# Optimization experiments

Measured on AMD Instinct MI355X. Metric: run time of the kernel, lower is better.

The kernel has to match this reference:

```python
import jax, jax.numpy as jnp
import numpy as np

C = 256; G = 8; K = 3; P = K * K; GC = C // G
PAD = K // 2; PAD_DW = 1
EPS_LN = 1e-5; EPS_DWLN = 1e-6; EPS_BN = 1e-5
OFFSET_SCALE = 1.0


def _ln(x, g, b, eps=EPS_LN):
    mu = x.mean(-1, keepdims=True)
    var = ((x - mu) ** 2).mean(-1, keepdims=True)
    return (x - mu) * jax.lax.rsqrt(var + eps) * g + b


def _bn(x, g, b, m, v):  # x: NCHW, eval-mode batchnorm with running stats
    s = jax.lax.rsqrt(v + EPS_BN)
    return (x - m[None, :, None, None]) * (g * s)[None, :, None, None] + b[None, :, None, None]


def _dcnv3_core(x, offset, mask):
    # x: (N,H,W,C) projected input; offset: (N,H,W,G*P*2); mask: (N,H,W,G,P) softmaxed
    N, H, W, _ = x.shape
    Hp, Wp = H + 2 * PAD, W + 2 * PAD
    x_pad = jnp.pad(x, ((0, 0), (PAD, PAD), (PAD, PAD), (0, 0)))
    img = x_pad.reshape(N, Hp, Wp, G, GC).transpose(0, 3, 4, 1, 2)  # (N,G,gc,Hp,Wp)
    # reference points, normalized by padded spatial dims (stride=1, dilation=1)
    start = (K - 1) // 2 + 0.5
    ref_x = (start + jnp.arange(W, dtype=x.dtype)) / Wp
    ref_y = (start + jnp.arange(H, dtype=x.dtype)) / Hp
    rx, ry = jnp.meshgrid(ref_x, ref_y, indexing='xy')  # (H,W)
    ref = jnp.stack([rx, ry], -1)  # (H,W,2) as (x,y)
    # dilation grid (kernel tap offsets), tap index p = i_w*K + j_h per torch meshgrid order
    gw = (jnp.arange(K, dtype=x.dtype) - (K - 1) // 2) / Wp
    gh = (jnp.arange(K, dtype=x.dtype) - (K - 1) // 2) / Hp
    gxx, gyy = jnp.meshgrid(gw, gh, indexing='ij')
    grid = jnp.stack([gxx, gyy], -1).reshape(P, 2)
    norm = jnp.array([Wp, Hp], dtype=x.dtype)
    off = offset.reshape(N, H, W, G, P, 2) * (OFFSET_SCALE / norm)
    loc = ref[None, :, :, None, None, :] + grid * OFFSET_SCALE + off  # (N,H,W,G,P,2)
    sg = (2.0 * loc - 1.0).transpose(0, 3, 1, 2, 4, 5).reshape(N, G, H * W, P, 2)

    def sample_one(im, gr):  # im: (gc,Hp,Wp), gr: (HW,P,2) in [-1,1]
        gx = (gr[..., 0] + 1.0) * (Wp / 2) - 0.5  # align_corners=False
        gy = (gr[..., 1] + 1.0) * (Hp / 2) - 0.5
        x0 = jnp.floor(gx); y0 = jnp.floor(gy)
        wx = gx - x0; wy = gy - y0
        def gat(ix, iy):
            valid = ((ix >= 0) & (ix <= Wp - 1) & (iy >= 0) & (iy <= Hp - 1)).astype(im.dtype)
            ixc = jnp.clip(ix, 0, Wp - 1).astype(jnp.int32)
            iyc = jnp.clip(iy, 0, Hp - 1).astype(jnp.int32)
            return im[:, iyc, ixc] * valid  # (gc,HW,P), zero padding outside
        return (gat(x0, y0) * ((1 - wx) * (1 - wy))
                + gat(x0 + 1, y0) * (wx * (1 - wy))
                + gat(x0, y0 + 1) * ((1 - wx) * wy)
                + gat(x0 + 1, y0 + 1) * (wx * wy))

    sampled = jax.vmap(jax.vmap(sample_one))(img, sg)  # (N,G,gc,HW,P)
    m = mask.transpose(0, 3, 1, 2, 4).reshape(N, G, 1, H * W, P)
    out = (sampled * m).sum(-1)  # (N,G,gc,HW)
    return out.transpose(0, 3, 1, 2).reshape(N, H, W, C)


def _dcnv3(inp, dw_w, dw_b, dwln_g, dwln_b, off_w, off_b, msk_w, msk_b, inp_w, inp_b, outp_w, outp_b):
    N, H, W, _ = inp.shape
    x = inp @ inp_w + inp_b  # input_proj
    # depthwise conv offset/mask branch (on the raw input, not the projection)
    x1 = jax.lax.conv_general_dilated(inp, dw_w, (1, 1), ((PAD_DW, PAD_DW), (PAD_DW, PAD_DW)),
                                      dimension_numbers=('NHWC', 'HWIO', 'NHWC'),
                                      feature_group_count=C) + dw_b
    x1 = jax.nn.gelu(_ln(x1, dwln_g, dwln_b, EPS_DWLN), approximate=False)
    offset = x1 @ off_w + off_b  # (N,H,W,G*P*2)
    mask = jax.nn.softmax((x1 @ msk_w + msk_b).reshape(N, H, W, G, P), axis=-1)
    return _dcnv3_core(x, offset, mask) @ outp_w + outp_b  # output_proj


def _forward(x, conv1_w, bn1_g, bn1_b, bn1_m, bn1_v, ln1_g, ln1_b, dw_w, dw_b, dwln_g, dwln_b,
             off_w, off_b, msk_w, msk_b, inp_w, inp_b, outp_w, outp_b, gamma1,
             ln2_g, ln2_b, fc1_w, fc1_b, fc2_w, fc2_b, gamma2, bn2_g, bn2_b, bn2_m, bn2_v):
    out = jax.lax.conv_general_dilated(x, conv1_w, (1, 1), ((1, 1), (1, 1)),
                                       dimension_numbers=('NCHW', 'OIHW', 'NCHW'))
    out = jax.nn.relu(_bn(out, bn1_g, bn1_b, bn1_m, bn1_v))
    t = out.transpose(0, 2, 3, 1)  # NHWC for the InternImage layer
    # post_norm InternImage layer with layer_scale
    d = _dcnv3(t, dw_w, dw_b, dwln_g, dwln_b, off_w, off_b, msk_w, msk_b, inp_w, inp_b, outp_w, outp_b)
    t = t + gamma1 * _ln(d, ln1_g, ln1_b)
    h = jax.nn.gelu(t @ fc1_w + fc1_b, approximate=False) @ fc2_w + fc2_b
    t = t + gamma2 * _ln(h, ln2_g, ln2_b)
    out = _bn(t.transpose(0, 3, 1, 2), bn2_g, bn2_b, bn2_m, bn2_v)
    return jax.nn.relu(out + x)  # residual (downsample is None: stride=1, inplanes==planes)


def setup_inputs() -> dict:
    key = jax.random.key(0)
    ks = iter(jax.random.split(key, 48))
    rn = lambda shape, s=1.0: jax.random.normal(next(ks), shape, dtype=jnp.float32) * s
    hid = 4 * C
    d = {}
    d['x'] = rn((8, C, 56, 56))
    d['conv1_w'] = rn((C, C, 3, 3), (2.0 / (9 * C)) ** 0.5)
    d['bn1_g'] = jnp.ones((C,), jnp.float32); d['bn1_b'] = jnp.zeros((C,), jnp.float32)
    d['bn1_m'] = rn((C,), 0.1)
    d['bn1_v'] = jax.random.uniform(next(ks), (C,), jnp.float32, 0.5, 1.5)
    d['ln1_g'] = jnp.ones((C,), jnp.float32); d['ln1_b'] = jnp.zeros((C,), jnp.float32)
    d['dw_w'] = rn((3, 3, 1, C), (1.0 / 9) ** 0.5); d['dw_b'] = jnp.zeros((C,), jnp.float32)
    d['dwln_g'] = jnp.ones((C,), jnp.float32); d['dwln_b'] = jnp.zeros((C,), jnp.float32)
    d['off_w'] = rn((C, G * P * 2), 0.01); d['off_b'] = rn((G * P * 2,), 0.01)
    d['msk_w'] = rn((C, G * P), 0.01); d['msk_b'] = jnp.zeros((G * P,), jnp.float32)
    d['inp_w'] = rn((C, C), C ** -0.5); d['inp_b'] = jnp.zeros((C,), jnp.float32)
    d['outp_w'] = rn((C, C), C ** -0.5); d['outp_b'] = jnp.zeros((C,), jnp.float32)
    d['gamma1'] = rn((C,), 0.01)
    d['ln2_g'] = jnp.ones((C,), jnp.float32); d['ln2_b'] = jnp.zeros((C,), jnp.float32)
    d['fc1_w'] = rn((C, hid), C ** -0.5); d['fc1_b'] = jnp.zeros((hid,), jnp.float32)
    d['fc2_w'] = rn((hid, C), hid ** -0.5); d['fc2_b'] = jnp.zeros((C,), jnp.float32)
    d['gamma2'] = rn((C,), 0.01)
    d['bn2_g'] = jnp.ones((C,), jnp.float32); d['bn2_b'] = jnp.zeros((C,), jnp.float32)
    d['bn2_m'] = rn((C,), 0.1)
    d['bn2_v'] = jax.random.uniform(next(ks), (C,), jnp.float32, 0.5, 1.5)
    return d


def reference(x, conv1_w, bn1_g, bn1_b, bn1_m, bn1_v, ln1_g, ln1_b, dw_w, dw_b, dwln_g, dwln_b,
              off_w, off_b, msk_w, msk_b, inp_w, inp_b, outp_w, outp_b, gamma1,
              ln2_g, ln2_b, fc1_w, fc1_b, fc2_w, fc2_b, gamma2, bn2_g, bn2_b, bn2_m, bn2_v):
    return _forward(x, conv1_w, bn1_g, bn1_b, bn1_m, bn1_v, ln1_g, ln1_b, dw_w, dw_b, dwln_g, dwln_b,
                    off_w, off_b, msk_w, msk_b, inp_w, inp_b, outp_w, outp_b, gamma1,
                    ln2_g, ln2_b, fc1_w, fc1_b, fc2_w, fc2_b, gamma2, bn2_g, bn2_b, bn2_m, bn2_v)
```

## Files before the change

kernel.cpp:

```cpp
#include <hip/hip_runtime.h>
#include <cmath>

#define N_   8
#define H_   56
#define W_   56
#define C_   256
#define HW_  3136
#define NHW_ 25088
#define G_   8
#define GC_  32
#define P_   9
#define HID_ 1024
#define XP_H 58
#define XP_W 58

typedef __attribute__((ext_vector_type(8))) short bf16x8;
typedef __attribute__((ext_vector_type(4))) float f32x4;

#define GLOAD_LDS16(g, l) __builtin_amdgcn_global_load_lds( \
    (const __attribute__((address_space(1))) void*)(g), \
    (__attribute__((address_space(3))) void*)(l), 16, 0, 0)

__device__ __forceinline__ unsigned short f2bf(float f) {
    unsigned u = __float_as_uint(f);
    u += 0x7FFF + ((u >> 16) & 1);
    return (unsigned short)(u >> 16);
}

__device__ __forceinline__ float gelu_exact(float v) {
    return 0.5f * v * (1.f + erff(v * 0.70710678118654752f));
}

__device__ __forceinline__ float2 block_sum2(float a, float b, float* sm) {
    int lane = threadIdx.x & 63;
    int wid  = threadIdx.x >> 6;
#pragma unroll
    for (int off = 32; off > 0; off >>= 1) {
        a += __shfl_down(a, off, 64);
        b += __shfl_down(b, off, 64);
    }
    if (lane == 0) { sm[wid] = a; sm[wid + 4] = b; }
    __syncthreads();
    float ra = sm[0] + sm[1] + sm[2] + sm[3];
    float rb = sm[4] + sm[5] + sm[6] + sm[7];
    __syncthreads();
    return make_float2(ra, rb);
}

__global__ __launch_bounds__(256) void k_prep_xpad(const float* __restrict__ x, unsigned short* __restrict__ xpad) {
    int nh = blockIdx.x;
    int n = nh / H_, h = nh - n * H_;
    int c = threadIdx.x;
    const float* xr = x + ((size_t)(n * C_ + c)) * HW_ + h * W_;
    unsigned short* orow = xpad + ((size_t)((n * XP_H + h + 1) * XP_W + 1)) * C_ + c;
    for (int w = 0; w < W_; ++w) orow[(size_t)w * C_] = f2bf(xr[w]);
}

__global__ __launch_bounds__(256) void k_prep_wTT(const float* __restrict__ w, unsigned short* __restrict__ wTT) {
    int i  = blockIdx.x * 256 + threadIdx.x;
    int ci = i & 255;
    int r  = i >> 8;
    int co = r & 255;
    int kk = r >> 8;
    wTT[i] = f2bf(w[(co * 256 + ci) * 9 + kk]);
}

__global__ __launch_bounds__(256) void k_prep_sqT(const float* __restrict__ src, unsigned short* __restrict__ dst) {
    int n = blockIdx.x, k = threadIdx.x;
    dst[n * C_ + k] = f2bf(src[k * C_ + n]);
}

__global__ __launch_bounds__(256) void k_prep_fc1T(const float* __restrict__ src, unsigned short* __restrict__ dst) {
    int n = blockIdx.x, k = threadIdx.x;
    dst[(size_t)n * C_ + k] = f2bf(src[(size_t)k * HID_ + n]);
}

__global__ __launch_bounds__(256) void k_prep_fc2T(const float* __restrict__ src, unsigned short* __restrict__ dst) {
    int n = blockIdx.x, k0 = threadIdx.x;
#pragma unroll
    for (int q = 0; q < 4; ++q) {
        int k = q * 256 + k0;
        dst[(size_t)n * HID_ + k] = f2bf(src[(size_t)k * C_ + n]);
    }
}

__global__ __launch_bounds__(256) void k_prep_om(const float* __restrict__ offw, const float* __restrict__ offb,
                                                 const float* __restrict__ mskw, const float* __restrict__ mskb,
                                                 unsigned short* __restrict__ omT, float* __restrict__ omb) {
    int n = blockIdx.x, k = threadIdx.x;
    float v = 0.f;
    if (n < 144)      v = offw[k * 144 + n];
    else if (n < 216) v = mskw[k * 72 + (n - 144)];
    omT[n * C_ + k] = f2bf(v);
    if (k == 0) omb[n] = (n < 144) ? offb[n] : (n < 216 ? mskb[n - 144] : 0.f);
}

__global__ __launch_bounds__(256) void k_conv1_mfma(const unsigned short* __restrict__ xpad,
                                                    const unsigned short* __restrict__ wTT,
                                                    const float* __restrict__ g, const float* __restrict__ b,
                                                    const float* __restrict__ m, const float* __restrict__ v,
                                                    float* __restrict__ t, unsigned short* __restrict__ t_bf) {
    __shared__ __align__(16) unsigned char smem[49152];
    unsigned short* sm16 = (unsigned short*)smem;
    int tid = threadIdx.x;
    int wave = tid >> 6, lane = tid & 63;
    int r = lane & 15, kq = lane >> 4;
    int mt = blockIdx.x >> 1, nt = blockIdx.x & 1;
    int m0 = mt * 64, n0 = nt * 128;
    int wm = wave & 1, wn = wave >> 1;

    int pix = m0 + wave * 16 + r;
    int n = pix / HW_, hw = pix - n * HW_;
    int h = hw / W_, w = hw - h * W_;
    size_t abase = ((size_t)((n * XP_H + h) * XP_W + w)) * C_;

    f32x4 acc[2][4] = {};

    auto stage = [&](int kt, int buf) {
        int tap = kt >> 2, ktk = kt & 3;
        int kh = tap / 3, kw = tap - kh * 3;
        int k0 = ktk * 64;
        unsigned short* dstA = sm16 + buf * 12288;
        unsigned short* dstB = dstA + 4096;
        const unsigned short* ap = xpad + abase + (size_t)(kh * XP_W + kw) * C_ + k0;
#pragma unroll
        for (int i = 0; i < 2; ++i)
            GLOAD_LDS16(ap + (i * 4 + kq) * 8, dstA + (wave * 2 + i) * 512);
#pragma unroll
        for (int i = 0; i < 4; ++i) {
            int q = wave * 4 + i;
            int nrow = n0 + (q >> 1) * 16 + r;
            int cc   = (q & 1) * 4 + kq;
            GLOAD_LDS16(wTT + ((size_t)(tap * C_) + nrow) * C_ + k0 + cc * 8, dstB + q * 512);
        }
    };

    stage(0, 0);
    int cur = 0;
#pragma unroll 1
    for (int kt = 0; kt < 36; ++kt) {
        if (kt < 35) {
            stage(kt + 1, cur ^ 1);
            asm volatile("s_waitcnt vmcnt(6)" ::: "memory");
        } else {
            asm volatile("s_waitcnt vmcnt(0)" ::: "memory");
        }
        __builtin_amdgcn_s_barrier();
        bf16x8* sA = (bf16x8*)(sm16 + cur * 12288);
        bf16x8* sB = sA + 512;
#pragma unroll
        for (int ks = 0; ks < 2; ++ks) {
            bf16x8 af[2], bfr[4];
#pragma unroll
            for (int mi = 0; mi < 2; ++mi) af[mi]  = sA[((wm * 2 + mi) * 2 + ks) * 64 + lane];
#pragma unroll
            for (int ni = 0; ni < 4; ++ni) bfr[ni] = sB[((wn * 4 + ni) * 2 + ks) * 64 + lane];
#pragma unroll
            for (int mi = 0; mi < 2; ++mi)
#pragma unroll
                for (int ni = 0; ni < 4; ++ni)
                    acc[mi][ni] = __builtin_amdgcn_mfma_f32_16x16x32_bf16(af[mi], bfr[ni], acc[mi][ni], 0, 0, 0);
        }
        __builtin_amdgcn_s_barrier();
        cur ^= 1;
    }

#pragma unroll
    for (int ni = 0; ni < 4; ++ni) {
        int co = n0 + (wn * 4 + ni) * 16 + r;
        float sc = g[co] * rsqrtf(v[co] + 1e-5f);
        float sh = b[co] - m[co] * sc;
#pragma unroll
        for (int mi = 0; mi < 2; ++mi) {
#pragma unroll
            for (int reg = 0; reg < 4; ++reg) {
                int po = m0 + (wm * 2 + mi) * 16 + kq * 4 + reg;
                float val = fmaxf(acc[mi][ni][reg] * sc + sh, 0.f);
                size_t idx = (size_t)po * C_ + co;
                t[idx] = val;
                t_bf[idx] = f2bf(val);
            }
        }
    }
}

__global__ __launch_bounds__(256) void k_inproj_mfma(const unsigned short* __restrict__ t_bf,
                                                     const unsigned short* __restrict__ inpwT,
                                                     const float* __restrict__ bias,
                                                     float* __restrict__ xproj) {
    __shared__ __align__(16) unsigned char smem[81920];
    unsigned short* sm16 = (unsigned short*)smem;
    int tid = threadIdx.x;
    int wave = tid >> 6, lane = tid & 63;
    int r = lane & 15, kq = lane >> 4;
    int m0 = blockIdx.x * 64;

    f32x4 acc[16] = {};

    auto stage = [&](int kt, int buf) {
        int k0 = kt * 64;
        unsigned short* dstA = sm16 + buf * 20480;
        unsigned short* dstB = dstA + 4096;
#pragma unroll
        for (int i = 0; i < 2; ++i) {
            int q = wave * 2 + i;
            int row = m0 + wave * 16 + r;
            GLOAD_LDS16(t_bf + (size_t)row * C_ + k0 + (i * 4 + kq) * 8, dstA + q * 512);
        }
#pragma unroll
        for (int i = 0; i < 8; ++i) {
            int q = wave * 8 + i;
            int nrow = (q >> 1) * 16 + r;
            int cc   = (q & 1) * 4 + kq;
            GLOAD_LDS16(inpwT + (size_t)nrow * C_ + k0 + cc * 8, dstB + q * 512);
        }
    };

    stage(0, 0);
    int cur = 0;
#pragma unroll 1
    for (int kt = 0; kt < 4; ++kt) {
        if (kt < 3) {
            stage(kt + 1, cur ^ 1);
            asm volatile("s_waitcnt vmcnt(10)" ::: "memory");
        } else {
            asm volatile("s_waitcnt vmcnt(0)" ::: "memory");
        }
        __builtin_amdgcn_s_barrier();
        bf16x8* sA = (bf16x8*)(sm16 + cur * 20480);
        bf16x8* sB = sA + 512;
#pragma unroll
        for (int ks = 0; ks < 2; ++ks) {
            bf16x8 a = sA[(wave * 2 + ks) * 64 + lane];
#pragma unroll
            for (int ni = 0; ni < 16; ++ni) {
                bf16x8 b = sB[(ni * 2 + ks) * 64 + lane];
                acc[ni] = __builtin_amdgcn_mfma_f32_16x16x32_bf16(a, b, acc[ni], 0, 0, 0);
            }
        }
        __builtin_amdgcn_s_barrier();
        cur ^= 1;
    }

#pragma unroll
    for (int ni = 0; ni < 16; ++ni) {
        int col = ni * 16 + r;
        float bb = bias[col];
#pragma unroll
        for (int reg = 0; reg < 4; ++reg) {
            int row = m0 + wave * 16 + kq * 4 + reg;
            xproj[(size_t)row * C_ + col] = acc[ni][reg] + bb;
        }
    }
}

__global__ __launch_bounds__(256) void k_dw(const float* __restrict__ t, const float* __restrict__ dww,
                                            const float* __restrict__ dwb, const float* __restrict__ lg,
                                            const float* __restrict__ lb, unsigned short* __restrict__ x1_bf) {
    __shared__ float sm[8];
    int pix = blockIdx.x;
    int n = pix / HW_, hw = pix - n * HW_;
    int h = hw / W_,  w = hw - h * W_;
    int c = threadIdx.x;
    float acc = dwb[c];
#pragma unroll
    for (int kh = 0; kh < 3; ++kh) {
        int y = h + kh - 1;
        if ((unsigned)y >= H_) continue;
#pragma unroll
        for (int kw = 0; kw < 3; ++kw) {
            int xx = w + kw - 1;
            if ((unsigned)xx >= W_) continue;
            acc = fmaf(t[(size_t)(n * HW_ + y * W_ + xx) * C_ + c], dww[(kh * 3 + kw) * C_ + c], acc);
        }
    }
    float2 r  = block_sum2(acc, acc * acc, sm);
    float mu  = r.x * (1.f / C_);
    float var = fmaxf(r.y * (1.f / C_) - mu * mu, 0.f);
    float rs  = rsqrtf(var + 1e-6f);
    float val = (acc - mu) * rs * lg[c] + lb[c];
    x1_bf[(size_t)pix * C_ + c] = f2bf(gelu_exact(val));
}

__global__ __launch_bounds__(256) void k_offmask_mfma(const unsigned short* __restrict__ x1_bf,
                                                      const unsigned short* __restrict__ omT,
                                                      const float* __restrict__ omb,
                                                      float* __restrict__ offo, float* __restrict__ msko) {
    __shared__ float som[32][225];
    int wave = threadIdx.x >> 6, lane = threadIdx.x & 63;
    int r = lane & 15, kq = lane >> 4;
    int p0 = blockIdx.x * 32, co0 = wave * 64;
    f32x4 acc[2][4] = {};
#pragma unroll 1
    for (int ks = 0; ks < 8; ++ks) {
        bf16x8 a0 = *(const bf16x8*)(x1_bf + (size_t)(p0 + r) * C_ + ks * 32 + kq * 8);
        bf16x8 a1 = *(const bf16x8*)(x1_bf + (size_t)(p0 + 16 + r) * C_ + ks * 32 + kq * 8);
        const unsigned short* bp = omT + (size_t)(co0 + r) * C_ + ks * 32 + kq * 8;
#pragma unroll
        for (int ni = 0; ni < 4; ++ni) {
            bf16x8 b = *(const bf16x8*)(bp + (size_t)ni * 16 * C_);
            acc[0][ni] = __builtin_amdgcn_mfma_f32_16x16x32_bf16(a0, b, acc[0][ni], 0, 0, 0);
            acc[1][ni] = __builtin_amdgcn_mfma_f32_16x16x32_bf16(a1, b, acc[1][ni], 0, 0, 0);
        }
    }
#pragma unroll
    for (int ni = 0; ni < 4; ++ni) {
        int col = co0 + ni * 16 + r;
        if (col < 216) {
            float bb = omb[col];
#pragma unroll
            for (int mi = 0; mi < 2; ++mi)
#pragma unroll
                for (int reg = 0; reg < 4; ++reg)
                    som[mi * 16 + kq * 4 + reg][col] = acc[mi][ni][reg] + bb;
        }
    }
    __syncthreads();
    int tid = threadIdx.x;
#pragma unroll
    for (int i = 0; i < 18; ++i) {
        int j = i * 256 + tid;
        int px = j / 144, col = j - px * 144;
        offo[(size_t)(p0 + px) * 144 + col] = som[px][col];
    }
    int px = tid >> 3, g = tid & 7;
    float mx = -1e30f;
#pragma unroll
    for (int p = 0; p < 9; ++p) mx = fmaxf(mx, som[px][144 + g * 9 + p]);
    float e[9], s = 0.f;
#pragma unroll
    for (int p = 0; p < 9; ++p) { e[p] = expf(som[px][144 + g * 9 + p] - mx); s += e[p]; }
    float inv = 1.f / s;
#pragma unroll
    for (int p = 0; p < 9; ++p) msko[(size_t)(p0 + px) * 72 + g * 9 + p] = e[p] * inv;
}

__global__ __launch_bounds__(256) void k_core(const float* __restrict__ xp,
                                              const float* __restrict__ offo, const float* __restrict__ msko,
                                              unsigned short* __restrict__ core_bf) {
    int pix = blockIdx.x;
    int n = pix / HW_, hw = pix - n * HW_;
    int h = hw / W_,  w = hw - h * W_;
    int g  = threadIdx.x >> 5;
    int cc = threadIdx.x & 31;
    const float* op = offo + (size_t)pix * 144 + g * 18;
    const float* mp = msko + (size_t)pix * 72 + g * 9;
    const float* xg = xp + (size_t)n * HW_ * C_ + g * GC_ + cc;
    float acc = 0.f;
#pragma unroll
    for (int p = 0; p < 9; ++p) {
        float gx = (float)(w + (p / 3)) + op[p * 2];
        float gy = (float)(h + (p % 3)) + op[p * 2 + 1];
        float fx = floorf(gx), fy = floorf(gy);
        float wx = gx - fx,   wy = gy - fy;
        int ix = (int)fx - 1, iy = (int)fy - 1;
        float v00 = 0.f, v10 = 0.f, v01 = 0.f, v11 = 0.f;
        bool x0ok = (unsigned)ix < W_, x1ok = (unsigned)(ix + 1) < W_;
        bool y0ok = (unsigned)iy < H_, y1ok = (unsigned)(iy + 1) < H_;
        if (y0ok) {
            const float* rr = xg + (size_t)(iy * W_) * C_;
            if (x0ok) v00 = rr[(size_t)ix * C_];
            if (x1ok) v10 = rr[(size_t)(ix + 1) * C_];
        }
        if (y1ok) {
            const float* rr = xg + (size_t)((iy + 1) * W_) * C_;
            if (x0ok) v01 = rr[(size_t)ix * C_];
            if (x1ok) v11 = rr[(size_t)(ix + 1) * C_];
        }
        float sval = (v00 * (1.f - wx) + v10 * wx) * (1.f - wy)
                   + (v01 * (1.f - wx) + v11 * wx) * wy;
        acc = fmaf(mp[p], sval, acc);
    }
    core_bf[(size_t)pix * C_ + threadIdx.x] = f2bf(acc);
}

__global__ __launch_bounds__(256) void k_outproj_mfma(const unsigned short* __restrict__ core_bf,
                                                      const unsigned short* __restrict__ outpwT,
                                                      const float* __restrict__ bo,
                                                      const float* __restrict__ g1, const float* __restrict__ lg,
                                                      const float* __restrict__ lb,
                                                      float* __restrict__ t, unsigned short* __restrict__ t_bf) {
    __shared__ float sd[32][260];
    int wave = threadIdx.x >> 6, lane = threadIdx.x & 63;
    int r = lane & 15, kq = lane >> 4;
    int p0 = blockIdx.x * 32, co0 = wave * 64;
    f32x4 acc[2][4] = {};
#pragma unroll 1
    for (int ks = 0; ks < 8; ++ks) {
        bf16x8 a0 = *(const bf16x8*)(core_bf + (size_t)(p0 + r) * C_ + ks * 32 + kq * 8);
        bf16x8 a1 = *(const bf16x8*)(core_bf + (size_t)(p0 + 16 + r) * C_ + ks * 32 + kq * 8);
        const unsigned short* bp = outpwT + (size_t)(co0 + r) * C_ + ks * 32 + kq * 8;
#pragma unroll
        for (int ni = 0; ni < 4; ++ni) {
            bf16x8 b = *(const bf16x8*)(bp + (size_t)ni * 16 * C_);
            acc[0][ni] = __builtin_amdgcn_mfma_f32_16x16x32_bf16(a0, b, acc[0][ni], 0, 0, 0);
            acc[1][ni] = __builtin_amdgcn_mfma_f32_16x16x32_bf16(a1, b, acc[1][ni], 0, 0, 0);
        }
    }
#pragma unroll
    for (int ni = 0; ni < 4; ++ni) {
        int col = co0 + ni * 16 + r;
        float bb = bo[col];
#pragma unroll
        for (int mi = 0; mi < 2; ++mi)
#pragma unroll
            for (int reg = 0; reg < 4; ++reg)
                sd[mi * 16 + kq * 4 + reg][col] = acc[mi][ni][reg] + bb;
    }
    __syncthreads();
    int px = threadIdx.x >> 3, sub = threadIdx.x & 7;
    float s1 = 0.f, s2 = 0.f;
#pragma unroll
    for (int i = 0; i < 8; ++i) {
        float4 vv = *(const float4*)&sd[px][sub * 32 + i * 4];
        s1 += vv.x + vv.y + vv.z + vv.w;
        s2 += vv.x * vv.x + vv.y * vv.y + vv.z * vv.z + vv.w * vv.w;
    }
#pragma unroll
    for (int off = 1; off < 8; off <<= 1) { s1 += __shfl_xor(s1, off, 64); s2 += __shfl_xor(s2, off, 64); }
    float mu  = s1 * (1.f / C_);
    float var = fmaxf(s2 * (1.f / C_) - mu * mu, 0.f);
    float rs  = rsqrtf(var + 1e-5f);
#pragma unroll
    for (int i = 0; i < 32; ++i) {
        int col = sub * 32 + i;
        size_t idx = (size_t)(p0 + px) * C_ + col;
        float tn = t[idx] + g1[col] * ((sd[px][col] - mu) * rs * lg[col] + lb[col]);
        t[idx] = tn;
        t_bf[idx] = f2bf(tn);
    }
}

__global__ __launch_bounds__(256) void k_fc1_mfma(const unsigned short* __restrict__ t_bf,
                                                  const unsigned short* __restrict__ fc1wT,
                                                  const float* __restrict__ fc1b,
                                                  unsigned short* __restrict__ h_bf) {
    __shared__ __align__(16) unsigned char smem[34816];
    unsigned short* sm16 = (unsigned short*)smem;
    bf16x8* sA = (bf16x8*)smem;
    bf16x8* sB = (bf16x8*)(smem + 16384);
    int tid = threadIdx.x;
    int wave = tid >> 6, lane = tid & 63;
    int r = lane & 15, kq = lane >> 4;
    int mt = blockIdx.x >> 3, nt = blockIdx.x & 7;
    int m0 = mt * 128, n0 = nt * 128;
    int wm = wave & 1, wn = wave >> 1;

    f32x4 acc[4][4] = {};
#pragma unroll 1
    for (int kt = 0; kt < 4; ++kt) {
        int k0 = kt * 64;
        if (kt) __syncthreads();
#pragma unroll
        for (int i = 0; i < 4; ++i) {
            int q = wave * 4 + i;
            int row = m0 + (q >> 1) * 16 + r;
            int cc  = (q & 1) * 4 + kq;
            GLOAD_LDS16(t_bf + (size_t)row * C_ + k0 + cc * 8, sm16 + q * 512);
        }
#pragma unroll
        for (int i = 0; i < 4; ++i) {
            int q = wave * 4 + i;
            int nrow = n0 + (q >> 1) * 16 + r;
            int cc   = (q & 1) * 4 + kq;
            GLOAD_LDS16(fc1wT + (size_t)nrow * C_ + k0 + cc * 8, sm16 + 8192 + q * 512);
        }
        __syncthreads();
#pragma unroll
        for (int ks = 0; ks < 2; ++ks) {
            bf16x8 af[4], bfr[4];
#pragma unroll
            for (int mi = 0; mi < 4; ++mi) af[mi]  = sA[((wm * 4 + mi) * 2 + ks) * 64 + lane];
#pragma unroll
            for (int ni = 0; ni < 4; ++ni) bfr[ni] = sB[((wn * 4 + ni) * 2 + ks) * 64 + lane];
#pragma unroll
            for (int mi = 0; mi < 4; ++mi)
#pragma unroll
                for (int ni = 0; ni < 4; ++ni)
                    acc[mi][ni] = __builtin_amdgcn_mfma_f32_16x16x32_bf16(af[mi], bfr[ni], acc[mi][ni], 0, 0, 0);
        }
    }
    __syncthreads();
#pragma unroll
    for (int ni = 0; ni < 4; ++ni) {
        int col = (wn * 4 + ni) * 16 + r;
        float bb = fc1b[n0 + col];
#pragma unroll
        for (int mi = 0; mi < 4; ++mi)
#pragma unroll
            for (int reg = 0; reg < 4; ++reg) {
                int row = (wm * 4 + mi) * 16 + kq * 4 + reg;
                sm16[row * 136 + col] = f2bf(gelu_exact(acc[mi][ni][reg] + bb));
            }
    }
    __syncthreads();
    int trow = tid >> 1, thalf = tid & 1;
    const unsigned short* src = sm16 + trow * 136 + thalf * 64;
    unsigned short* dst = h_bf + (size_t)(m0 + trow) * HID_ + n0 + thalf * 64;
#pragma unroll
    for (int j = 0; j < 8; ++j)
        *(bf16x8*)(dst + j * 8) = *(const bf16x8*)(src + j * 8);
}

__global__ __launch_bounds__(256) void k_fc2ln_mfma(const unsigned short* __restrict__ h_bf,
                                                    const unsigned short* __restrict__ fc2wT,
                                                    const float* __restrict__ fc2b,
                                                    const float* __restrict__ g2, const float* __restrict__ lg,
                                                    const float* __restrict__ lb, float* __restrict__ t) {
    __shared__ __align__(16) unsigned char smem[81920];
    unsigned short* sm16 = (unsigned short*)smem;
    int tid = threadIdx.x;
    int wave = tid >> 6, lane = tid & 63;
    int r = lane & 15, kq = lane >> 4;
    int m0 = blockIdx.x * 64;

    f32x4 acc[16] = {};

    auto stage = [&](int kt, int buf) {
        int k0 = kt * 64;
        unsigned short* dstA = sm16 + buf * 20480;
        unsigned short* dstB = dstA + 4096;
#pragma unroll
        for (int i = 0; i < 2; ++i) {
            int q = wave * 2 + i;
            int row = m0 + wave * 16 + r;
            GLOAD_LDS16(h_bf + (size_t)row * HID_ + k0 + (i * 4 + kq) * 8, dstA + q * 512);
        }
#pragma unroll
        for (int i = 0; i < 8; ++i) {
            int q = wave * 8 + i;
            int nrow = (q >> 1) * 16 + r;
            int cc   = (q & 1) * 4 + kq;
            GLOAD_LDS16(fc2wT + (size_t)nrow * HID_ + k0 + cc * 8, dstB + q * 512);
        }
    };

    stage(0, 0);
    int cur = 0;
#pragma unroll 1
    for (int kt = 0; kt < 16; ++kt) {
        if (kt < 15) {
            stage(kt + 1, cur ^ 1);
            asm volatile("s_waitcnt vmcnt(10)" ::: "memory");
        } else {
            asm volatile("s_waitcnt vmcnt(0)" ::: "memory");
        }
        __builtin_amdgcn_s_barrier();
        bf16x8* sA = (bf16x8*)(sm16 + cur * 20480);
        bf16x8* sB = sA + 512;
#pragma unroll
        for (int ks = 0; ks < 2; ++ks) {
            bf16x8 a = sA[(wave * 2 + ks) * 64 + lane];
#pragma unroll
            for (int ni = 0; ni < 16; ++ni) {
                bf16x8 b = sB[(ni * 2 + ks) * 64 + lane];
                acc[ni] = __builtin_amdgcn_mfma_f32_16x16x32_bf16(a, b, acc[ni], 0, 0, 0);
            }
        }
        __builtin_amdgcn_s_barrier();
        cur ^= 1;
    }
    float bb[16], g2v[16], lgv[16], lbv[16];
#pragma unroll
    for (int ni = 0; ni < 16; ++ni) {
        int col = ni * 16 + r;
        bb[ni] = fc2b[col]; g2v[ni] = g2[col]; lgv[ni] = lg[col]; lbv[ni] = lb[col];
    }
#pragma unroll
    for (int ni = 0; ni < 16; ++ni)
#pragma unroll
        for (int reg = 0; reg < 4; ++reg) acc[ni][reg] += bb[ni];
#pragma unroll
    for (int reg = 0; reg < 4; ++reg) {
        float s1 = 0.f, s2 = 0.f;
#pragma unroll
        for (int ni = 0; ni < 16; ++ni) { float vv = acc[ni][reg]; s1 += vv; s2 += vv * vv; }
#pragma unroll
        for (int off = 1; off < 16; off <<= 1) { s1 += __shfl_xor(s1, off, 64); s2 += __shfl_xor(s2, off, 64); }
        float mu  = s1 * (1.f / C_);
        float var = fmaxf(s2 * (1.f / C_) - mu * mu, 0.f);
        float rs  = rsqrtf(var + 1e-5f);
        int row = m0 + wave * 16 + kq * 4 + reg;
        float* tr = t + (size_t)row * C_;
#pragma unroll
        for (int ni = 0; ni < 16; ++ni) {
            int col = ni * 16 + r;
            tr[col] += g2v[ni] * ((acc[ni][reg] - mu) * rs * lgv[ni] + lbv[ni]);
        }
    }
}

__global__ __launch_bounds__(256) void k_final(const float* __restrict__ t, const float* __restrict__ x,
                                               const float* __restrict__ g, const float* __restrict__ b,
                                               const float* __restrict__ m, const float* __restrict__ v,
                                               float* __restrict__ out) {
    int i  = blockIdx.x * 256 + threadIdx.x;
    int hw = i % HW_;
    int r  = i / HW_;
    int c  = r & 255;
    int n  = r >> 8;
    float tv  = t[(size_t)(n * HW_ + hw) * C_ + c];
    float s   = rsqrtf(v[c] + 1e-5f);
    float val = (tv - m[c]) * (g[c] * s) + b[c] + x[i];
    out[i] = fmaxf(val, 0.f);
}

extern "C" void kernel_launch(void* const* d_in, const int* in_sizes, int n_in,
                              void* d_out, int out_size, void* d_ws, size_t ws_size,
                              hipStream_t stream) {
    const float* x      = (const float*)d_in[0];
    const float* conv1w = (const float*)d_in[1];
    const float* bn1g   = (const float*)d_in[2];
    const float* bn1b   = (const float*)d_in[3];
    const float* bn1m   = (const float*)d_in[4];
    const float* bn1v   = (const float*)d_in[5];
    const float* ln1g   = (const float*)d_in[6];
    const float* ln1b   = (const float*)d_in[7];
    const float* dww    = (const float*)d_in[8];
    const float* dwb    = (const float*)d_in[9];
    const float* dwlng  = (const float*)d_in[10];
    const float* dwlnb  = (const float*)d_in[11];
    const float* offw   = (const float*)d_in[12];
    const float* offb   = (const float*)d_in[13];
    const float* mskw   = (const float*)d_in[14];
    const float* mskb   = (const float*)d_in[15];
    const float* inpw   = (const float*)d_in[16];
    const float* inpb   = (const float*)d_in[17];
    const float* outpw  = (const float*)d_in[18];
    const float* outpb  = (const float*)d_in[19];
    const float* gamma1 = (const float*)d_in[20];
    const float* ln2g   = (const float*)d_in[21];
    const float* ln2b   = (const float*)d_in[22];
    const float* fc1w   = (const float*)d_in[23];
    const float* fc1b   = (const float*)d_in[24];
    const float* fc2w   = (const float*)d_in[25];
    const float* fc2b   = (const float*)d_in[26];
    const float* gamma2 = (const float*)d_in[27];
    const float* bn2g   = (const float*)d_in[28];
    const float* bn2b   = (const float*)d_in[29];
    const float* bn2m   = (const float*)d_in[30];
    const float* bn2v   = (const float*)d_in[31];
    float* out = (float*)d_out;

    float* ws    = (float*)d_ws;
    float* xproj = ws;
    float* offo  = xproj + (size_t)NHW_ * C_;
    float* msko  = offo  + (size_t)NHW_ * 144;
    unsigned short* x1_bf = (unsigned short*)(msko + (size_t)NHW_ * 72);
    unsigned short* scr   = x1_bf + (size_t)NHW_ * C_;
    float* t     = (float*)(scr + (size_t)N_ * XP_H * XP_W * C_);
    float* omb   = t + (size_t)NHW_ * C_;
    unsigned short* t_bf  = (unsigned short*)(omb + 256);
    unsigned short* wTT   = t_bf  + (size_t)NHW_ * C_;
    unsigned short* inpwT = wTT   + (size_t)9 * C_ * C_;
    unsigned short* outpwT= inpwT + (size_t)C_ * C_;
    unsigned short* fc1wT = outpwT+ (size_t)C_ * C_;
    unsigned short* fc2wT = fc1wT + (size_t)HID_ * C_;
    unsigned short* omT   = fc2wT + (size_t)C_ * HID_;
    unsigned short* xpad    = scr;
    unsigned short* core_bf = scr;
    unsigned short* h_bf    = (unsigned short*)xproj;

    hipMemsetAsync(xpad, 0, (size_t)N_ * XP_H * XP_W * C_ * sizeof(unsigned short), stream);
    k_prep_xpad<<<N_ * H_, 256, 0, stream>>>(x, xpad);
    k_prep_wTT <<<2304,    256, 0, stream>>>(conv1w, wTT);
    k_prep_sqT <<<256,     256, 0, stream>>>(inpw, inpwT);
    k_prep_sqT <<<256,     256, 0, stream>>>(outpw, outpwT);
    k_prep_fc1T<<<1024,    256, 0, stream>>>(fc1w, fc1wT);
    k_prep_fc2T<<<256,     256, 0, stream>>>(fc2w, fc2wT);
    k_prep_om  <<<256,     256, 0, stream>>>(offw, offb, mskw, mskb, omT, omb);

    k_conv1_mfma  <<<(NHW_ / 64) * 2, 256, 0, stream>>>(xpad, wTT, bn1g, bn1b, bn1m, bn1v, t, t_bf);
    k_inproj_mfma <<<NHW_ / 64, 256, 0, stream>>>(t_bf, inpwT, inpb, xproj);
    k_dw          <<<NHW_,      256, 0, stream>>>(t, dww, dwb, dwlng, dwlnb, x1_bf);
    k_offmask_mfma<<<NHW_ / 32, 256, 0, stream>>>(x1_bf, omT, omb, offo, msko);
    k_core        <<<NHW_,      256, 0, stream>>>(xproj, offo, msko, core_bf);
    k_outproj_mfma<<<NHW_ / 32, 256, 0, stream>>>(core_bf, outpwT, outpb, gamma1, ln1g, ln1b, t, t_bf);
    k_fc1_mfma    <<<(NHW_ / 128) * 8, 256, 0, stream>>>(t_bf, fc1wT, fc1b, h_bf);
    k_fc2ln_mfma  <<<NHW_ / 64, 256, 0, stream>>>(h_bf, fc2wT, fc2b, gamma2, ln2g, ln2b, t);
    k_final       <<<NHW_,      256, 0, stream>>>(t, x, bn2g, bn2b, bn2m, bn2v, out);
}
```

Measured before the change: 647.0 us.

## Fuse final BN2/residual/ReLU into fc2 kernel and swizzle conv1 block order

Merges the final batchnorm, residual add and ReLU into the fc2+LayerNorm kernel. The tile result is staged in shared memory and transposed so the NCHW output is written directly, which avoids writing the intermediate t back and re-reading it in a separate kernel. It also remaps conv1 block indices so consecutive blocks spread over M tiles, aiming for better cache locality. The shared-memory transpose adds a barrier, and the serial loop over channels may limit store throughput.

```diff
diff --git a/kernel.cpp b/kernel.cpp
--- a/kernel.cpp
+++ b/kernel.cpp
@@ -105,7 +105,9 @@
     int tid = threadIdx.x;
     int wave = tid >> 6, lane = tid & 63;
     int r = lane & 15, kq = lane >> 4;
-    int mt = blockIdx.x >> 1, nt = blockIdx.x & 1;
+    int bid = blockIdx.x;
+    int swz = (bid & 7) * 98 + (bid >> 3);
+    int mt = swz >> 1, nt = swz & 1;
     int m0 = mt * 64, n0 = nt * 128;
     int wm = wave & 1, wn = wave >> 1;
 
@@ -502,11 +504,15 @@
         *(bf16x8*)(dst + j * 8) = *(const bf16x8*)(src + j * 8);
 }
 
-__global__ __launch_bounds__(256) void k_fc2ln_mfma(const unsigned short* __restrict__ h_bf,
-                                                    const unsigned short* __restrict__ fc2wT,
-                                                    const float* __restrict__ fc2b,
-                                                    const float* __restrict__ g2, const float* __restrict__ lg,
-                                                    const float* __restrict__ lb, float* __restrict__ t) {
+__global__ __launch_bounds__(256) void k_fc2fin_mfma(const unsigned short* __restrict__ h_bf,
+                                                     const unsigned short* __restrict__ fc2wT,
+                                                     const float* __restrict__ fc2b,
+                                                     const float* __restrict__ g2, const float* __restrict__ lg,
+                                                     const float* __restrict__ lb, const float* __restrict__ t,
+                                                     const float* __restrict__ x,
+                                                     const float* __restrict__ bn2g, const float* __restrict__ bn2b,
+                                                     const float* __restrict__ bn2m, const float* __restrict__ bn2v,
+                                                     float* __restrict__ out) {
     __shared__ __align__(16) unsigned char smem[81920];
     unsigned short* sm16 = (unsigned short*)smem;
     int tid = threadIdx.x;
@@ -560,6 +566,8 @@
         __builtin_amdgcn_s_barrier();
         cur ^= 1;
     }
+
+    float* ot = (float*)smem;
     float bb[16], g2v[16], lgv[16], lbv[16];
 #pragma unroll
     for (int ni = 0; ni < 16; ++ni) {
@@ -580,29 +588,27 @@
         float mu  = s1 * (1.f / C_);
         float var = fmaxf(s2 * (1.f / C_) - mu * mu, 0.f);
         float rs  = rsqrtf(var + 1e-5f);
-        int row = m0 + wave * 16 + kq * 4 + reg;
-        float* tr = t + (size_t)row * C_;
+        int row_local = wave * 16 + kq * 4 + reg;
+        const float* tr = t + (size_t)(m0 + row_local) * C_;
 #pragma unroll
         for (int ni = 0; ni < 16; ++ni) {
             int col = ni * 16 + r;
-            tr[col] += g2v[ni] * ((acc[ni][reg] - mu) * rs * lgv[ni] + lbv[ni]);
-        }
-    }
-}
-
-__global__ __launch_bounds__(256) void k_final(const float* __restrict__ t, const float* __restrict__ x,
-                                               const float* __restrict__ g, const float* __restrict__ b,
-                                               const float* __restrict__ m, const float* __restrict__ v,
-                                               float* __restrict__ out) {
-    int i  = blockIdx.x * 256 + threadIdx.x;
-    int hw = i % HW_;
-    int r  = i / HW_;
-    int c  = r & 255;
-    int n  = r >> 8;
-    float tv  = t[(size_t)(n * HW_ + hw) * C_ + c];
-    float s   = rsqrtf(v[c] + 1e-5f);
-    float val = (tv - m[c]) * (g[c] * s) + b[c] + x[i];
-    out[i] = fmaxf(val, 0.f);
+            ot[row_local * 257 + col] = tr[col] + g2v[ni] * ((acc[ni][reg] - mu) * rs * lgv[ni] + lbv[ni]);
+        }
+    }
+    __syncthreads();
+
+    int n  = m0 / HW_;
+    int hw0 = m0 - n * HW_;
+#pragma unroll 1
+    for (int i = 0; i < 64; ++i) {
+        int c = wave * 64 + i;
+        float sc = bn2g[c] * rsqrtf(bn2v[c] + 1e-5f);
+        float sh = bn2b[c] - bn2m[c] * sc;
+        size_t gidx = ((size_t)(n * C_ + c)) * HW_ + hw0 + lane;
+        float val = ot[lane * 257 + c] * sc + sh + x[gidx];
+        out[gidx] = fmaxf(val, 0.f);
+    }
 }
 
 extern "C" void kernel_launch(void* const* d_in, const int* in_sizes, int n_in,
@@ -677,6 +683,6 @@
     k_core        <<<NHW_,      256, 0, stream>>>(xproj, offo, msko, core_bf);
     k_outproj_mfma<<<NHW_ / 32, 256, 0, stream>>>(core_bf, outpwT, outpb, gamma1, ln1g, ln1b, t, t_bf);
     k_fc1_mfma    <<<(NHW_ / 128) * 8, 256, 0, stream>>>(t_bf, fc1wT, fc1b, h_bf);
-    k_fc2ln_mfma  <<<NHW_ / 64, 256, 0, stream>>>(h_bf, fc2wT, fc2b, gamma2, ln2g, ln2b, t);
-    k_final       <<<NHW_,      256, 0, stream>>>(t, x, bn2g, bn2b, bn2m, bn2v, out);
-}
+    k_fc2fin_mfma <<<NHW_ / 64, 256, 0, stream>>>(h_bf, fc2wT, fc2b, gamma2, ln2g, ln2b, t,
+                                                  x, bn2g, bn2b, bn2m, bn2v, out);
+}
```

New measurement: 625.0 us. 3.4% less time.
